# Optimization experiments

Measured on AMD Instinct MI355X. Metric: run time of the kernel, lower is better.

Reference implementation:

```python
import jax, jax.numpy as jnp
import numpy as np


def setup_inputs() -> dict:
    key = jax.random.key(0)
    ks = jax.random.split(key, 5)
    B, T, D, H = 64, 1024, 512, 1024
    s = 1.0 / np.sqrt(H)
    return {
        "x": jax.random.normal(ks[0], (B, T, D), dtype=jnp.float32),
        "W_ih": jax.random.normal(ks[1], (3 * H, D), dtype=jnp.float32) * s,
        "W_hh": jax.random.normal(ks[2], (3 * H, H), dtype=jnp.float32) * s,
        "b_ih": jax.random.normal(ks[3], (3 * H,), dtype=jnp.float32) * s,
        "b_hh": jax.random.normal(ks[4], (3 * H,), dtype=jnp.float32) * s,
    }


def reference(x, W_ih, W_hh, b_ih, b_hh):
    # GRULayer: per-timestep GRU cell recurrence, zero initial hidden state.
    B, T, D = x.shape
    H = W_hh.shape[1]
    h0 = jnp.zeros((B, H), dtype=x.dtype)
    xT = jnp.swapaxes(x, 0, 1)  # [T, B, D]

    def step(h, x_t):
        gi = x_t @ W_ih.T + b_ih          # [B, 3H]
        gh = h @ W_hh.T + b_hh            # [B, 3H]
        i_r, i_z, i_n = jnp.split(gi, 3, axis=-1)
        h_r, h_z, h_n = jnp.split(gh, 3, axis=-1)
        r = jax.nn.sigmoid(i_r + h_r)
        z = jax.nn.sigmoid(i_z + h_z)
        n = jnp.tanh(i_n + r * h_n)
        h_new = (1.0 - z) * n + z * h
        return h_new, h_new

    h_final, outs = jax.lax.scan(step, h0, xT)  # outs: [T, B, H]
    res = jnp.swapaxes(outs, 0, 1)              # [B, T, H]
    return res, h_final
```

## Files before the change

kernel.cpp:

```cpp
#include <hip/hip_runtime.h>
#include <hip/hip_bf16.h>

#define NB 64
#define TT 1024
#define ND 512
#define NH 1024
#define GRID 256
#define NTH 256

typedef float f32x4 __attribute__((ext_vector_type(4)));
typedef __bf16 bf16x8 __attribute__((ext_vector_type(8)));

__device__ __forceinline__ float sigmoid_f(float v) { return 1.0f / (1.0f + __expf(-v)); }

__device__ __forceinline__ float tanh_f(float v) {
    float a = fabsf(v);
    float e = __expf(-2.0f * a);
    float t = (1.0f - e) / (1.0f + e);
    return copysignf(t, v);
}

__device__ __forceinline__ f32x4 load_dwordx4_sc1(const void* p) {
    f32x4 r;
    asm volatile("global_load_dwordx4 %0, %1, off sc1" : "=v"(r) : "v"(p));
    return r;
}
__device__ __forceinline__ void store_short_sc1(void* p, unsigned v16) {
    asm volatile("global_store_short %0, %1, off sc1" :: "v"(p), "v"(v16) : "memory");
}
__device__ __forceinline__ void store_dword_sc1(unsigned* p, unsigned v) {
    asm volatile("global_store_dword %0, %1, off sc1" :: "v"(p), "v"(v) : "memory");
}
__device__ __forceinline__ unsigned load_dword_sc1_wait(const unsigned* p) {
    unsigned v;
    asm volatile("global_load_dword %0, %1, off sc1\n\ts_waitcnt vmcnt(0)"
                 : "=v"(v) : "v"(p) : "memory");
    return v;
}

__global__ void __launch_bounds__(NTH) gru_kernel(
    const float* __restrict__ x, const float* __restrict__ W_ih,
    const float* __restrict__ W_hh, const float* __restrict__ b_ih,
    const float* __restrict__ b_hh, float* __restrict__ out,
    unsigned* __restrict__ flags, __bf16* __restrict__ hbuf)
{
    extern __shared__ char smem[];
    __bf16* WihF = (__bf16*)smem;
    __bf16* WhhF = WihF + 4 * 4 * 3 * 64 * 8;
    float* prz = (float*)(WhhF + 4 * 8 * 3 * 64 * 8);
    float* pnx = prz + 2048;
    float* pnh = pnx + 1024;

    const int tid = threadIdx.x;
    const int bg = blockIdx.x >> 6;
    const int cg = blockIdx.x & 63;
    const int brow = bg << 4;
    const int hc0 = cg << 4;

    for (int s = tid; s < 4 * 4 * 3 * 64; s += NTH) {
        int lane = s & 63, r = s >> 6;
        int g = r % 3, r2 = r / 3;
        int it = r2 & 3, w = r2 >> 2;
        int k = w * 128 + it * 32 + (lane >> 4) * 8;
        int col = lane & 15;
        const float* src = W_ih + (size_t)(g * NH + hc0 + col) * ND + k;
        float4 va = *(const float4*)(src);
        float4 vb = *(const float4*)(src + 4);
        bf16x8 f;
        f[0] = (__bf16)va.x; f[1] = (__bf16)va.y; f[2] = (__bf16)va.z; f[3] = (__bf16)va.w;
        f[4] = (__bf16)vb.x; f[5] = (__bf16)vb.y; f[6] = (__bf16)vb.z; f[7] = (__bf16)vb.w;
        *(bf16x8*)(WihF + (size_t)s * 8) = f;
    }
    for (int s = tid; s < 4 * 8 * 3 * 64; s += NTH) {
        int lane = s & 63, r = s >> 6;
        int g = r % 3, r2 = r / 3;
        int it = r2 & 7, w = r2 >> 3;
        int k = w * 256 + it * 32 + (lane >> 4) * 8;
        int col = lane & 15;
        const float* src = W_hh + (size_t)(g * NH + hc0 + col) * NH + k;
        float4 va = *(const float4*)(src);
        float4 vb = *(const float4*)(src + 4);
        bf16x8 f;
        f[0] = (__bf16)va.x; f[1] = (__bf16)va.y; f[2] = (__bf16)va.z; f[3] = (__bf16)va.w;
        f[4] = (__bf16)vb.x; f[5] = (__bf16)vb.y; f[6] = (__bf16)vb.z; f[7] = (__bf16)vb.w;
        *(bf16x8*)(WhhF + (size_t)s * 8) = f;
    }

    const int jcol = tid & 15;
    const int mrow = tid >> 4;
    const float b_r = b_ih[hc0 + jcol] + b_hh[hc0 + jcol];
    const float b_z = b_ih[NH + hc0 + jcol] + b_hh[NH + hc0 + jcol];
    const float b_nx = b_ih[2 * NH + hc0 + jcol];
    const float b_nh = b_hh[2 * NH + hc0 + jcol];

    __syncthreads();

    const int wave = tid >> 6;
    const int lane = tid & 63;
    const int lrow = lane & 15;
    const int kgrp = lane >> 4;

    unsigned* myflag = flags + ((size_t)(bg * 64 + cg)) * 16;
    const unsigned* pollflag = flags + ((size_t)(bg * 64 + (tid & 63))) * 16;

    __bf16* hst0 = hbuf + (size_t)NB * NH + (size_t)(brow + mrow) * NH + hc0 + jcol;
    __bf16* hst1 = hbuf + (size_t)(brow + mrow) * NH + hc0 + jcol;

    float hp = 0.0f;

    f32x4 xa[4], xb[4];
    {
        const float* xr = x + ((size_t)(brow + lrow) * TT + 0) * ND + wave * 128 + kgrp * 8;
        #pragma unroll
        for (int it = 0; it < 4; ++it) {
            xa[it] = *(const f32x4*)(xr + it * 32);
            xb[it] = *(const f32x4*)(xr + it * 32 + 4);
        }
    }

    int p = 0;
    for (int t = 0; t < TT; ++t) {
        f32x4 ar{}, az{}, anx{}, anh{};

        #pragma unroll
        for (int it = 0; it < 4; ++it) {
            bf16x8 af;
            af[0] = (__bf16)xa[it][0]; af[1] = (__bf16)xa[it][1];
            af[2] = (__bf16)xa[it][2]; af[3] = (__bf16)xa[it][3];
            af[4] = (__bf16)xb[it][0]; af[5] = (__bf16)xb[it][1];
            af[6] = (__bf16)xb[it][2]; af[7] = (__bf16)xb[it][3];
            const __bf16* wp = WihF + ((size_t)(wave * 4 + it) * 3) * 512 + lane * 8;
            bf16x8 wr = *(const bf16x8*)(wp);
            bf16x8 wz = *(const bf16x8*)(wp + 512);
            bf16x8 wn = *(const bf16x8*)(wp + 1024);
            ar  = __builtin_amdgcn_mfma_f32_16x16x32_bf16(af, wr, ar, 0, 0, 0);
            az  = __builtin_amdgcn_mfma_f32_16x16x32_bf16(af, wz, az, 0, 0, 0);
            anx = __builtin_amdgcn_mfma_f32_16x16x32_bf16(af, wn, anx, 0, 0, 0);
        }

        if (t > 0) {
            if (tid < 64) {
                const unsigned tgt = (unsigned)t;
                for (;;) {
                    unsigned v = load_dword_sc1_wait(pollflag);
                    if (__all(v >= tgt)) break;
                }
            }
            __syncthreads();
        }

        const __bf16* hrow = hbuf + (size_t)p * NB * NH + (size_t)(brow + lrow) * NH
                           + wave * 256 + kgrp * 8;
        f32x4 hraw[8];
        #pragma unroll
        for (int it = 0; it < 8; ++it)
            hraw[it] = load_dwordx4_sc1(hrow + it * 32);
        asm volatile("s_waitcnt vmcnt(0)" ::: "memory");
        __builtin_amdgcn_sched_barrier(0);
        #pragma unroll
        for (int it = 0; it < 8; ++it) {
            bf16x8 af = __builtin_bit_cast(bf16x8, hraw[it]);
            const __bf16* wp = WhhF + ((size_t)(wave * 8 + it) * 3) * 512 + lane * 8;
            bf16x8 wr = *(const bf16x8*)(wp);
            bf16x8 wz = *(const bf16x8*)(wp + 512);
            bf16x8 wn = *(const bf16x8*)(wp + 1024);
            ar  = __builtin_amdgcn_mfma_f32_16x16x32_bf16(af, wr, ar, 0, 0, 0);
            az  = __builtin_amdgcn_mfma_f32_16x16x32_bf16(af, wz, az, 0, 0, 0);
            anh = __builtin_amdgcn_mfma_f32_16x16x32_bf16(af, wn, anh, 0, 0, 0);
        }

        if (t + 1 < TT) {
            const float* xn = x + ((size_t)(brow + lrow) * TT + (t + 1)) * ND
                            + wave * 128 + kgrp * 8;
            #pragma unroll
            for (int it = 0; it < 4; ++it) {
                xa[it] = *(const f32x4*)(xn + it * 32);
                xb[it] = *(const f32x4*)(xn + it * 32 + 4);
            }
        }

        #pragma unroll
        for (int j = 0; j < 4; ++j) {
            int row = kgrp * 4 + j;
            prz[wave * 512 + row * 32 + lrow]      = ar[j];
            prz[wave * 512 + row * 32 + 16 + lrow] = az[j];
            pnx[wave * 256 + row * 16 + lrow]      = anx[j];
            pnh[wave * 256 + row * 16 + lrow]      = anh[j];
        }
        __syncthreads();

        {
            float rpre = prz[mrow * 32 + jcol] + prz[512 + mrow * 32 + jcol]
                       + prz[1024 + mrow * 32 + jcol] + prz[1536 + mrow * 32 + jcol] + b_r;
            float zpre = prz[mrow * 32 + 16 + jcol] + prz[512 + mrow * 32 + 16 + jcol]
                       + prz[1024 + mrow * 32 + 16 + jcol] + prz[1536 + mrow * 32 + 16 + jcol] + b_z;
            float ginn = pnx[mrow * 16 + jcol] + pnx[256 + mrow * 16 + jcol]
                       + pnx[512 + mrow * 16 + jcol] + pnx[768 + mrow * 16 + jcol] + b_nx;
            float ghnn = pnh[mrow * 16 + jcol] + pnh[256 + mrow * 16 + jcol]
                       + pnh[512 + mrow * 16 + jcol] + pnh[768 + mrow * 16 + jcol] + b_nh;
            float r = sigmoid_f(rpre);
            float z = sigmoid_f(zpre);
            float n = tanh_f(ginn + r * ghnn);
            float hn = (1.0f - z) * n + z * hp;
            hp = hn;
            out[((size_t)(brow + mrow) * TT + t) * NH + hc0 + jcol] = hn;
            unsigned hb = (unsigned)__builtin_bit_cast(unsigned short, (__bf16)hn);
            store_short_sc1(p ? hst1 : hst0, hb);
            if (t == TT - 1)
                out[(size_t)NB * TT * NH + (size_t)(brow + mrow) * NH + hc0 + jcol] = hn;
        }

        if (t < TT - 1) {
            asm volatile("s_waitcnt vmcnt(0)" ::: "memory");
            __syncthreads();
            if (tid == 0)
                store_dword_sc1(myflag, (unsigned)(t + 1));
        }
        p ^= 1;
    }
}

extern "C" void kernel_launch(void* const* d_in, const int* in_sizes, int n_in,
                              void* d_out, int out_size, void* d_ws, size_t ws_size,
                              hipStream_t stream) {
    (void)in_sizes; (void)n_in; (void)out_size;
    const float* x    = (const float*)d_in[0];
    const float* W_ih = (const float*)d_in[1];
    const float* W_hh = (const float*)d_in[2];
    const float* b_ih = (const float*)d_in[3];
    const float* b_hh = (const float*)d_in[4];
    float* out = (float*)d_out;

    unsigned* flags = (unsigned*)d_ws;
    __bf16* hbuf = (__bf16*)((char*)d_ws + 16384);
    const size_t clear_bytes = 16384 + (size_t)NB * NH * sizeof(__bf16);
    if (ws_size < 16384 + (size_t)2 * NB * NH * sizeof(__bf16)) return;
    hipMemsetAsync(d_ws, 0, clear_bytes, stream);

    const size_t smem_bytes = 163840;
    (void)hipFuncSetAttribute((const void*)gru_kernel,
                              hipFuncAttributeMaxDynamicSharedMemorySize, (int)smem_bytes);
    gru_kernel<<<GRID, NTH, smem_bytes, stream>>>(x, W_ih, W_hh, b_ih, b_hh, out, flags, hbuf);
}
```

Measured before the change: 3.686 ms.

## Replace block-level flag barrier with per-wave tags and per-wave polling

Each wave now publishes its own completion tag right after storing its slice of the hidden state, instead of the whole block waiting on a __syncthreads before one thread sets a flag. Each wave also polls only the 16 producer blocks whose hidden columns it consumes, so waves can start their W_hh MFMAs independently without a block barrier. The h store and tag store are moved ahead of the large fp32 output store, and an s_sleep is added in the poll loop. The change relies on an exact-equality tag check and a trailing __syncthreads for LDS reuse, and adds four times as many tags to poll.

```diff
diff --git a/kernel.cpp b/kernel.cpp
--- a/kernel.cpp
+++ b/kernel.cpp
@@ -42,7 +42,7 @@
     const float* __restrict__ x, const float* __restrict__ W_ih,
     const float* __restrict__ W_hh, const float* __restrict__ b_ih,
     const float* __restrict__ b_hh, float* __restrict__ out,
-    unsigned* __restrict__ flags, __bf16* __restrict__ hbuf)
+    unsigned* __restrict__ tags, __bf16* __restrict__ hbuf)
 {
     extern __shared__ char smem[];
     __bf16* WihF = (__bf16*)smem;
@@ -58,11 +58,11 @@
     const int hc0 = cg << 4;
 
     for (int s = tid; s < 4 * 4 * 3 * 64; s += NTH) {
-        int lane = s & 63, r = s >> 6;
+        int ln = s & 63, r = s >> 6;
         int g = r % 3, r2 = r / 3;
         int it = r2 & 3, w = r2 >> 2;
-        int k = w * 128 + it * 32 + (lane >> 4) * 8;
-        int col = lane & 15;
+        int k = w * 128 + it * 32 + (ln >> 4) * 8;
+        int col = ln & 15;
         const float* src = W_ih + (size_t)(g * NH + hc0 + col) * ND + k;
         float4 va = *(const float4*)(src);
         float4 vb = *(const float4*)(src + 4);
@@ -72,11 +72,11 @@
         *(bf16x8*)(WihF + (size_t)s * 8) = f;
     }
     for (int s = tid; s < 4 * 8 * 3 * 64; s += NTH) {
-        int lane = s & 63, r = s >> 6;
+        int ln = s & 63, r = s >> 6;
         int g = r % 3, r2 = r / 3;
         int it = r2 & 7, w = r2 >> 3;
-        int k = w * 256 + it * 32 + (lane >> 4) * 8;
-        int col = lane & 15;
+        int k = w * 256 + it * 32 + (ln >> 4) * 8;
+        int col = ln & 15;
         const float* src = W_hh + (size_t)(g * NH + hc0 + col) * NH + k;
         float4 va = *(const float4*)(src);
         float4 vb = *(const float4*)(src + 4);
@@ -100,8 +100,8 @@
     const int lrow = lane & 15;
     const int kgrp = lane >> 4;
 
-    unsigned* myflag = flags + ((size_t)(bg * 64 + cg)) * 16;
-    const unsigned* pollflag = flags + ((size_t)(bg * 64 + (tid & 63))) * 16;
+    unsigned* mytag = tags + ((size_t)(bg * 64 + cg) * 16 + wave);
+    const unsigned* polltag = tags + ((size_t)(bg * 64 + wave * 16 + (lane >> 2)) * 16 + (lane & 3));
 
     __bf16* hst0 = hbuf + (size_t)NB * NH + (size_t)(brow + mrow) * NH + hc0 + jcol;
     __bf16* hst1 = hbuf + (size_t)(brow + mrow) * NH + hc0 + jcol;
@@ -118,8 +118,8 @@
         }
     }
 
-    int p = 0;
     for (int t = 0; t < TT; ++t) {
+        const int par = t & 1;
         f32x4 ar{}, az{}, anx{}, anh{};
 
         #pragma unroll
@@ -139,17 +139,15 @@
         }
 
         if (t > 0) {
-            if (tid < 64) {
-                const unsigned tgt = (unsigned)t;
-                for (;;) {
-                    unsigned v = load_dword_sc1_wait(pollflag);
-                    if (__all(v >= tgt)) break;
-                }
+            const unsigned tgt = (unsigned)t;
+            for (;;) {
+                unsigned v = load_dword_sc1_wait(polltag);
+                if (__all(v == tgt)) break;
+                __builtin_amdgcn_s_sleep(1);
             }
-            __syncthreads();
-        }
-
-        const __bf16* hrow = hbuf + (size_t)p * NB * NH + (size_t)(brow + lrow) * NH
+        }
+
+        const __bf16* hrow = hbuf + (size_t)par * NB * NH + (size_t)(brow + lrow) * NH
                            + wave * 256 + kgrp * 8;
         f32x4 hraw[8];
         #pragma unroll
@@ -203,20 +201,19 @@
             float n = tanh_f(ginn + r * ghnn);
             float hn = (1.0f - z) * n + z * hp;
             hp = hn;
+
+            unsigned hb = (unsigned)__builtin_bit_cast(unsigned short, (__bf16)hn);
+            store_short_sc1(par ? hst1 : hst0, hb);
+            asm volatile("s_waitcnt vmcnt(0)" ::: "memory");
+            if (t < TT - 1 && lane == 0)
+                store_dword_sc1(mytag, (unsigned)(t + 1));
+
             out[((size_t)(brow + mrow) * TT + t) * NH + hc0 + jcol] = hn;
-            unsigned hb = (unsigned)__builtin_bit_cast(unsigned short, (__bf16)hn);
-            store_short_sc1(p ? hst1 : hst0, hb);
             if (t == TT - 1)
                 out[(size_t)NB * TT * NH + (size_t)(brow + mrow) * NH + hc0 + jcol] = hn;
         }
 
-        if (t < TT - 1) {
-            asm volatile("s_waitcnt vmcnt(0)" ::: "memory");
-            __syncthreads();
-            if (tid == 0)
-                store_dword_sc1(myflag, (unsigned)(t + 1));
-        }
-        p ^= 1;
+        __syncthreads();
     }
 }
 
@@ -231,7 +228,7 @@
     const float* b_hh = (const float*)d_in[4];
     float* out = (float*)d_out;
 
-    unsigned* flags = (unsigned*)d_ws;
+    unsigned* tags = (unsigned*)d_ws;
     __bf16* hbuf = (__bf16*)((char*)d_ws + 16384);
     const size_t clear_bytes = 16384 + (size_t)NB * NH * sizeof(__bf16);
     if (ws_size < 16384 + (size_t)2 * NB * NH * sizeof(__bf16)) return;
@@ -240,5 +237,5 @@
     const size_t smem_bytes = 163840;
     (void)hipFuncSetAttribute((const void*)gru_kernel,
                               hipFuncAttributeMaxDynamicSharedMemorySize, (int)smem_bytes);
-    gru_kernel<<<GRID, NTH, smem_bytes, stream>>>(x, W_ih, W_hh, b_ih, b_hh, out, flags, hbuf);
-}
+    gru_kernel<<<GRID, NTH, smem_bytes, stream>>>(x, W_ih, W_hh, b_ih, b_hh, out, tags, hbuf);
+}
```

New measurement: 3.751 ms. About the same (+1.8%).
